# Kernel tuning notes

Measured on AMD Instinct MI355X. Metric: run time of the kernel, lower is better.

The kernel has to match this reference:

```python
import jax, jax.numpy as jnp
import numpy as np

IN_FEATURES = 4096
OUT_FEATURES = 11008
B, S = 4, 2048


def setup_inputs() -> dict:
    key = jax.random.key(0)
    k1, k2, k3, k4 = jax.random.split(key, 4)
    x = jax.random.normal(k1, (B, S, IN_FEATURES), dtype=jnp.float32)
    # packed uint8 bytes (two int4 nibbles per byte), stored as int32 in [0,256)
    qweight_packed = jax.random.randint(k2, (OUT_FEATURES, IN_FEATURES // 2), 0, 256, dtype=jnp.int32)
    # row-wise symmetric scales (positive, small)
    w_scales = jax.random.uniform(k3, (OUT_FEATURES, 1), dtype=jnp.float32) * 0.01 + 1e-4
    bias = jax.random.normal(k4, (OUT_FEATURES,), dtype=jnp.float32)
    return {"x": x, "qweight_packed": qweight_packed, "w_scales": w_scales, "bias": bias}


def _dequant(qweight_packed, w_scales, k_orig):
    # unpack two 4-bit nibbles per byte: low nibble first, then high nibble
    u = qweight_packed.astype(jnp.uint8)
    low = (u & 15).astype(jnp.int32)
    high = ((u >> 4) & 15).astype(jnp.int32)
    full = jnp.stack([low, high], axis=-1).reshape(u.shape[0], -1)[:, :k_orig]  # [N, K]
    w_int4 = jnp.where(full > 7, full - 16, full).astype(jnp.float32)
    return w_int4 * w_scales.astype(jnp.float32)  # [N, K]


def reference(x, qweight_packed, w_scales, bias):
    k = x.shape[-1]
    w = _dequant(qweight_packed, w_scales, k).astype(x.dtype)  # [N, K]
    x2 = x.reshape(-1, k)
    y2 = x2 @ w.T + bias.astype(x.dtype)
    return y2.reshape(*x.shape[:-1], w.shape[0])
```

## Files before the change

kernel.cpp:

```cpp
#include <hip/hip_runtime.h>
#include <stdint.h>

#define M_DIM 8192
#define N_DIM 11008
#define K_DIM 4096
#define KB_PACK 2048

#define BM 128
#define BN 128
#define BK 64

typedef __attribute__((ext_vector_type(4))) int   i32x4;
typedef __attribute__((ext_vector_type(4))) float f32x4;

__device__ __forceinline__ void gload_lds16(const int8_t* g, int8_t* l) {
    __builtin_amdgcn_global_load_lds(
        (const __attribute__((address_space(1))) void*)g,
        (__attribute__((address_space(3))) void*)l,
        16, 0, 0);
}

__global__ __launch_bounds__(256) void quant_x_kernel(const float* __restrict__ x,
                                                      int8_t* __restrict__ xq,
                                                      float* __restrict__ xs) {
    const int m   = blockIdx.x;
    const int tid = threadIdx.x;
    const float4* row = (const float4*)(x + (size_t)m * K_DIM);

    float4 v[4];
    float amax = 0.f;
#pragma unroll
    for (int i = 0; i < 4; ++i) {
        v[i] = row[i * 256 + tid];
        amax = fmaxf(amax, fmaxf(fmaxf(fabsf(v[i].x), fabsf(v[i].y)),
                                 fmaxf(fabsf(v[i].z), fabsf(v[i].w))));
    }
#pragma unroll
    for (int off = 32; off > 0; off >>= 1)
        amax = fmaxf(amax, __shfl_xor(amax, off));
    __shared__ float red[4];
    if ((tid & 63) == 0) red[tid >> 6] = amax;
    __syncthreads();
    amax = fmaxf(fmaxf(red[0], red[1]), fmaxf(red[2], red[3]));

    const float safe = fmaxf(amax, 1e-20f);
    const float inv  = 127.f / safe;
    if (tid == 0) xs[m] = safe * (1.f / 127.f);

    int* out = (int*)(xq + (size_t)m * K_DIM);
#pragma unroll
    for (int i = 0; i < 4; ++i) {
        int c0 = __float2int_rn(v[i].x * inv);
        int c1 = __float2int_rn(v[i].y * inv);
        int c2 = __float2int_rn(v[i].z * inv);
        int c3 = __float2int_rn(v[i].w * inv);
        out[i * 256 + tid] = (c0 & 255) | ((c1 & 255) << 8) | ((c2 & 255) << 16) | (c3 << 24);
    }
}

__device__ __forceinline__ int unpack2(int v0, int v1) {
    int l0 = (((v0 & 15) ^ 8) - 8) & 255;
    int h0 = ((((v0 >> 4) & 15) ^ 8) - 8) & 255;
    int l1 = (((v1 & 15) ^ 8) - 8) & 255;
    int h1 = ((((v1 >> 4) & 15) ^ 8) - 8) & 255;
    return l0 | (h0 << 8) | (l1 << 16) | (h1 << 24);
}

__global__ __launch_bounds__(256) void unpack_w_kernel(const int* __restrict__ qw,
                                                       int8_t* __restrict__ wq) {
    size_t i = (size_t)blockIdx.x * 256 + threadIdx.x;
    const i32x4* q4 = (const i32x4*)qw;
    i32x4 a = q4[2 * i];
    i32x4 b = q4[2 * i + 1];
    i32x4 o;
    o.x = unpack2(a.x, a.y);
    o.y = unpack2(a.z, a.w);
    o.z = unpack2(b.x, b.y);
    o.w = unpack2(b.z, b.w);
    ((i32x4*)wq)[i] = o;
}

__global__ __launch_bounds__(256) void gemm_i8_kernel(
    const int8_t* __restrict__ A,
    const int8_t* __restrict__ B,
    const float* __restrict__ xs,
    const float* __restrict__ wsc,
    const float* __restrict__ bias,
    float* __restrict__ C) {
    __shared__ int8_t As[BM * BK];
    __shared__ int8_t Bs[BN * BK];

    const int tid  = threadIdx.x;
    const int lane = tid & 63;
    const int wid  = tid >> 6;
    const int wm   = (wid >> 1) * 64;
    const int wn   = (wid & 1) * 64;
    const int m0   = blockIdx.y * BM;
    const int n0   = blockIdx.x * BN;

    const int r   = tid >> 2;
    const int c16 = (tid & 3) * 16;
    const int8_t* ga0 = A + (size_t)(m0 + r) * K_DIM + c16;
    const int8_t* ga1 = A + (size_t)(m0 + r + 64) * K_DIM + c16;
    const int8_t* gb0 = B + (size_t)(n0 + r) * K_DIM + c16;
    const int8_t* gb1 = B + (size_t)(n0 + r + 64) * K_DIM + c16;
    int8_t* la0 = As + r * BK + c16;
    int8_t* la1 = As + (r + 64) * BK + c16;
    int8_t* lb0 = Bs + r * BK + c16;
    int8_t* lb1 = Bs + (r + 64) * BK + c16;

    const int l15  = lane & 15;
    const int kq16 = (lane >> 4) * 16;

    i32x4 acc[4][4] = {};

    for (int k0 = 0; k0 < K_DIM; k0 += BK) {
        gload_lds16(ga0 + k0, la0);
        gload_lds16(ga1 + k0, la1);
        gload_lds16(gb0 + k0, lb0);
        gload_lds16(gb1 + k0, lb1);
        __syncthreads();

        i32x4 af[4], bfr[4];
#pragma unroll
        for (int i = 0; i < 4; ++i) {
            af[i]  = *(const i32x4*)(As + (wm + i * 16 + l15) * BK + kq16);
            bfr[i] = *(const i32x4*)(Bs + (wn + i * 16 + l15) * BK + kq16);
        }
#pragma unroll
        for (int mi = 0; mi < 4; ++mi)
#pragma unroll
            for (int ni = 0; ni < 4; ++ni)
                acc[mi][ni] = __builtin_amdgcn_mfma_i32_16x16x64_i8(
                    af[mi], bfr[ni], acc[mi][ni], 0, 0, 0);
        __syncthreads();
    }

    const int row0 = (lane >> 4) * 4;
    float sm[4][4];
#pragma unroll
    for (int mi = 0; mi < 4; ++mi)
#pragma unroll
        for (int ri = 0; ri < 4; ++ri)
            sm[mi][ri] = xs[m0 + wm + mi * 16 + row0 + ri];

#pragma unroll
    for (int ni = 0; ni < 4; ++ni) {
        int n = n0 + wn + ni * 16 + l15;
        float sn = wsc[n];
        float bv = bias[n];
#pragma unroll
        for (int mi = 0; mi < 4; ++mi) {
#pragma unroll
            for (int ri = 0; ri < 4; ++ri) {
                int m = m0 + wm + mi * 16 + row0 + ri;
                C[(size_t)m * N_DIM + n] = (float)acc[mi][ni][ri] * (sm[mi][ri] * sn) + bv;
            }
        }
    }
}

__global__ void fallback_kernel(const float* __restrict__ x, const int* __restrict__ qw,
                                const float* __restrict__ sc, const float* __restrict__ bias,
                                float* __restrict__ y) {
    int m = blockIdx.y;
    int n = blockIdx.x * 256 + threadIdx.x;
    __shared__ float xsh[K_DIM];
    for (int k = threadIdx.x; k < K_DIM; k += 256) xsh[k] = x[(size_t)m * K_DIM + k];
    __syncthreads();
    if (n < N_DIM) {
        float acc = 0.f;
        const int* qr = qw + (size_t)n * KB_PACK;
        for (int kb = 0; kb < KB_PACK; ++kb) {
            int v = qr[kb] & 255;
            int lo = v & 15; lo -= (lo & 8) << 1;
            int hi = (v >> 4) & 15; hi -= (hi & 8) << 1;
            acc += xsh[2 * kb] * (float)lo + xsh[2 * kb + 1] * (float)hi;
        }
        y[(size_t)m * N_DIM + n] = acc * sc[n] + bias[n];
    }
}

extern "C" void kernel_launch(void* const* d_in, const int* in_sizes, int n_in,
                              void* d_out, int out_size, void* d_ws, size_t ws_size,
                              hipStream_t stream) {
    const float* x    = (const float*)d_in[0];
    const int*   qw   = (const int*)d_in[1];
    const float* sc   = (const float*)d_in[2];
    const float* bias = (const float*)d_in[3];
    float*       y    = (float*)d_out;

    const size_t xq_bytes = (size_t)M_DIM * K_DIM;
    const size_t wq_bytes = (size_t)N_DIM * K_DIM;
    const size_t xs_bytes = (size_t)M_DIM * sizeof(float);
    const size_t need = xq_bytes + wq_bytes + xs_bytes;

    if (ws_size >= need) {
        int8_t* xq = (int8_t*)d_ws;
        int8_t* wq = xq + xq_bytes;
        float*  xs = (float*)(wq + wq_bytes);
        quant_x_kernel<<<M_DIM, 256, 0, stream>>>(x, xq, xs);
        unpack_w_kernel<<<(int)((size_t)N_DIM * K_DIM / 16 / 256), 256, 0, stream>>>(qw, wq);
        gemm_i8_kernel<<<dim3(N_DIM / BN, M_DIM / BM), 256, 0, stream>>>(xq, wq, xs, sc, bias, y);
    } else {
        fallback_kernel<<<dim3((N_DIM + 255) / 256, M_DIM), 256, 0, stream>>>(x, qw, sc, bias, y);
    }
}
```

Baseline: 1.043 ms.

## Rewrite int8 GEMM with 256x256 tiles, double-buffered swizzled LDS and interleaved staging

The int8 MFMA GEMM moves from 128x128x64 tiles with 256 threads to 256x256x128 tiles with 512 threads and a 128KB double-buffered LDS. Global-to-LDS loads for the next K tiles are interleaved between MFMA groups using explicit barriers, vmcnt waits and s_setprio. An XOR swizzle on the LDS layout is meant to avoid bank conflicts, and a block-index remap is meant to improve L2 reuse. The cost is heavy LDS use that allows only one block per CU, plus a fragile hand-written waitcnt and barrier schedule.

```diff
diff --git a/kernel.cpp b/kernel.cpp
--- a/kernel.cpp
+++ b/kernel.cpp
@@ -6,9 +6,11 @@
 #define K_DIM 4096
 #define KB_PACK 2048
 
-#define BM 128
-#define BN 128
-#define BK 64
+#define BM 256
+#define BN 256
+#define BK 128
+#define NKT (K_DIM / BK)
+#define THREADS 512
 
 typedef __attribute__((ext_vector_type(4))) int   i32x4;
 typedef __attribute__((ext_vector_type(4))) float f32x4;
@@ -80,84 +82,142 @@
     ((i32x4*)wq)[i] = o;
 }
 
-__global__ __launch_bounds__(256) void gemm_i8_kernel(
+__global__ __launch_bounds__(THREADS, 2) void gemm_i8_kernel(
     const int8_t* __restrict__ A,
     const int8_t* __restrict__ B,
     const float* __restrict__ xs,
     const float* __restrict__ wsc,
     const float* __restrict__ bias,
     float* __restrict__ C) {
-    __shared__ int8_t As[BM * BK];
-    __shared__ int8_t Bs[BN * BK];
+    __shared__ int8_t lds[131072];
 
     const int tid  = threadIdx.x;
     const int lane = tid & 63;
     const int wid  = tid >> 6;
-    const int wm   = (wid >> 1) * 64;
-    const int wn   = (wid & 1) * 64;
-    const int m0   = blockIdx.y * BM;
-    const int n0   = blockIdx.x * BN;
-
-    const int r   = tid >> 2;
-    const int c16 = (tid & 3) * 16;
-    const int8_t* ga0 = A + (size_t)(m0 + r) * K_DIM + c16;
-    const int8_t* ga1 = A + (size_t)(m0 + r + 64) * K_DIM + c16;
-    const int8_t* gb0 = B + (size_t)(n0 + r) * K_DIM + c16;
-    const int8_t* gb1 = B + (size_t)(n0 + r + 64) * K_DIM + c16;
-    int8_t* la0 = As + r * BK + c16;
-    int8_t* la1 = As + (r + 64) * BK + c16;
-    int8_t* lb0 = Bs + r * BK + c16;
-    int8_t* lb1 = Bs + (r + 64) * BK + c16;
-
+    const int wr   = wid >> 2;
+    const int wc   = wid & 3;
     const int l15  = lane & 15;
-    const int kq16 = (lane >> 4) * 16;
-
-    i32x4 acc[4][4] = {};
-
-    for (int k0 = 0; k0 < K_DIM; k0 += BK) {
-        gload_lds16(ga0 + k0, la0);
-        gload_lds16(ga1 + k0, la1);
-        gload_lds16(gb0 + k0, lb0);
-        gload_lds16(gb1 + k0, lb1);
-        __syncthreads();
-
-        i32x4 af[4], bfr[4];
-#pragma unroll
-        for (int i = 0; i < 4; ++i) {
-            af[i]  = *(const i32x4*)(As + (wm + i * 16 + l15) * BK + kq16);
-            bfr[i] = *(const i32x4*)(Bs + (wn + i * 16 + l15) * BK + kq16);
+    const int q    = lane >> 4;
+
+    const int lin = blockIdx.y * gridDim.x + blockIdx.x;
+    const int swz = (lin & 7) * 172 + (lin >> 3);
+    const int m0  = (swz & 31) * BM;
+    const int n0  = (swz >> 5) * BN;
+
+    const int sr   = tid >> 2;
+    const int scol = (((tid & 3) ^ ((tid >> 3) & 3)) << 4);
+    const int8_t* gA = A + (size_t)(m0 + sr) * K_DIM + scol;
+    const int8_t* gB = B + (size_t)(n0 + sr) * K_DIM + scol;
+    const int sdst = tid * 16;
+
+#define STAGE_A(KT, S) do { \
+        const int8_t* g_ = gA + (size_t)(KT) * BK + (S) * 64; \
+        int8_t* d_ = lds + (((KT) & 1) << 15) + ((S) << 14) + sdst; \
+        gload_lds16(g_, d_); \
+        gload_lds16(g_ + (size_t)128 * K_DIM, d_ + 8192); \
+    } while (0)
+#define STAGE_B(KT, S) do { \
+        const int8_t* g_ = gB + (size_t)(KT) * BK + (S) * 64; \
+        int8_t* d_ = lds + 65536 + (((KT) & 1) << 15) + ((S) << 14) + sdst; \
+        gload_lds16(g_, d_); \
+        gload_lds16(g_ + (size_t)128 * K_DIM, d_ + 8192); \
+    } while (0)
+
+    const int fswz = ((q ^ ((l15 >> 1) & 3)) << 4);
+    const int aoff = (wr * 128 + l15) * 64 + fswz;
+    const int boff = 65536 + (wc * 64 + l15) * 64 + fswz;
+
+#define LDA(MI, SS, BS) (*(const i32x4*)(lds + (aoff + (BS) + (SS) * 16384 + (MI) * 1024)))
+#define LDB(NI, SS, BS) (*(const i32x4*)(lds + (boff + (BS) + (SS) * 16384 + (NI) * 1024)))
+#define MFMA(D, AOP, BOP) D = __builtin_amdgcn_mfma_i32_16x16x64_i8(AOP, BOP, D, 0, 0, 0)
+
+    i32x4 acc[8][4] = {};
+
+    STAGE_A(0, 0); STAGE_B(0, 0); STAGE_A(0, 1); STAGE_B(0, 1);
+    STAGE_A(1, 0); STAGE_B(1, 0); STAGE_A(1, 1);
+    asm volatile("s_waitcnt vmcnt(6)" ::: "memory");
+    __builtin_amdgcn_s_barrier();
+
+    for (int kt = 0; kt < NKT; ++kt) {
+        const int bsel = (kt & 1) << 15;
+        const int s1 = (kt + 1 < NKT) ? kt + 1 : kt - 1;
+        const int s2 = (kt + 2 < NKT) ? kt + 2 : kt;
+        i32x4 af[8], bf0, bf1, bf2, bf3;
+
+#pragma unroll
+        for (int mi = 0; mi < 8; ++mi) af[mi] = LDA(mi, 0, bsel);
+        bf0 = LDB(0, 0, bsel);
+        bf1 = LDB(1, 0, bsel);
+        STAGE_B(s1, 1);
+        __builtin_amdgcn_s_barrier();
+        __builtin_amdgcn_s_setprio(1);
+#pragma unroll
+        for (int mi = 0; mi < 8; ++mi) { MFMA(acc[mi][0], af[mi], bf0); MFMA(acc[mi][1], af[mi], bf1); }
+        __builtin_amdgcn_s_setprio(0);
+        __builtin_amdgcn_s_barrier();
+
+        bf2 = LDB(2, 0, bsel);
+        bf3 = LDB(3, 0, bsel);
+        STAGE_A(s2, 0);
+        __builtin_amdgcn_s_barrier();
+        __builtin_amdgcn_s_setprio(1);
+#pragma unroll
+        for (int mi = 0; mi < 8; ++mi) { MFMA(acc[mi][2], af[mi], bf2); MFMA(acc[mi][3], af[mi], bf3); }
+        __builtin_amdgcn_s_setprio(0);
+        __builtin_amdgcn_s_barrier();
+
+#pragma unroll
+        for (int mi = 0; mi < 8; ++mi) af[mi] = LDA(mi, 1, bsel);
+        bf0 = LDB(0, 1, bsel);
+        bf1 = LDB(1, 1, bsel);
+        STAGE_B(s2, 0);
+        __builtin_amdgcn_s_barrier();
+        __builtin_amdgcn_s_setprio(1);
+#pragma unroll
+        for (int mi = 0; mi < 8; ++mi) { MFMA(acc[mi][0], af[mi], bf0); MFMA(acc[mi][1], af[mi], bf1); }
+        __builtin_amdgcn_s_setprio(0);
+        __builtin_amdgcn_s_barrier();
+
+        bf2 = LDB(2, 1, bsel);
+        bf3 = LDB(3, 1, bsel);
+        STAGE_A(s2, 1);
+        __builtin_amdgcn_s_barrier();
+        __builtin_amdgcn_s_setprio(1);
+#pragma unroll
+        for (int mi = 0; mi < 8; ++mi) { MFMA(acc[mi][2], af[mi], bf2); MFMA(acc[mi][3], af[mi], bf3); }
+        __builtin_amdgcn_s_setprio(0);
+        asm volatile("s_waitcnt vmcnt(6)" ::: "memory");
+        __builtin_amdgcn_s_barrier();
+    }
+
+    const int row0 = q * 4;
+    float sn[4], bv[4];
+#pragma unroll
+    for (int ni = 0; ni < 4; ++ni) {
+        const int n = n0 + wc * 64 + ni * 16 + l15;
+        sn[ni] = wsc[n];
+        bv[ni] = bias[n];
+    }
+#pragma unroll
+    for (int mi = 0; mi < 8; ++mi) {
+        const int mbase = m0 + wr * 128 + mi * 16 + row0;
+        float sm[4];
+#pragma unroll
+        for (int ri = 0; ri < 4; ++ri) sm[ri] = xs[mbase + ri];
+#pragma unroll
+        for (int ni = 0; ni < 4; ++ni) {
+            const int n = n0 + wc * 64 + ni * 16 + l15;
+            float* cp = C + (size_t)mbase * N_DIM + n;
+#pragma unroll
+            for (int ri = 0; ri < 4; ++ri)
+                cp[(size_t)ri * N_DIM] = (float)acc[mi][ni][ri] * (sm[ri] * sn[ni]) + bv[ni];
         }
-#pragma unroll
-        for (int mi = 0; mi < 4; ++mi)
-#pragma unroll
-            for (int ni = 0; ni < 4; ++ni)
-                acc[mi][ni] = __builtin_amdgcn_mfma_i32_16x16x64_i8(
-                    af[mi], bfr[ni], acc[mi][ni], 0, 0, 0);
-        __syncthreads();
-    }
-
-    const int row0 = (lane >> 4) * 4;
-    float sm[4][4];
-#pragma unroll
-    for (int mi = 0; mi < 4; ++mi)
-#pragma unroll
-        for (int ri = 0; ri < 4; ++ri)
-            sm[mi][ri] = xs[m0 + wm + mi * 16 + row0 + ri];
-
-#pragma unroll
-    for (int ni = 0; ni < 4; ++ni) {
-        int n = n0 + wn + ni * 16 + l15;
-        float sn = wsc[n];
-        float bv = bias[n];
-#pragma unroll
-        for (int mi = 0; mi < 4; ++mi) {
-#pragma unroll
-            for (int ri = 0; ri < 4; ++ri) {
-                int m = m0 + wm + mi * 16 + row0 + ri;
-                C[(size_t)m * N_DIM + n] = (float)acc[mi][ni][ri] * (sm[mi][ri] * sn) + bv;
-            }
-        }
-    }
+    }
+#undef STAGE_A
+#undef STAGE_B
+#undef LDA
+#undef LDB
+#undef MFMA
 }
 
 __global__ void fallback_kernel(const float* __restrict__ x, const int* __restrict__ qw,
@@ -201,7 +261,7 @@
         float*  xs = (float*)(wq + wq_bytes);
         quant_x_kernel<<<M_DIM, 256, 0, stream>>>(x, xq, xs);
         unpack_w_kernel<<<(int)((size_t)N_DIM * K_DIM / 16 / 256), 256, 0, stream>>>(qw, wq);
-        gemm_i8_kernel<<<dim3(N_DIM / BN, M_DIM / BM), 256, 0, stream>>>(xq, wq, xs, sc, bias, y);
+        gemm_i8_kernel<<<dim3(N_DIM / BN, M_DIM / BM), THREADS, 0, stream>>>(xq, wq, xs, sc, bias, y);
     } else {
         fallback_kernel<<<dim3((N_DIM + 255) / 256, M_DIM), 256, 0, stream>>>(x, qw, sc, bias, y);
     }
```

Result: faster. 885.0 us (-15.1%).
